# Performance work log

Hardware: AMD Instinct MI355X
Metric: run time of the kernel (lower is better)

Reference implementation:

```python
import jax, jax.numpy as jnp
import numpy as np

N_FILTERS = 40
FILTER_SIZE = 401   # int(16000*25/1000), forced odd
POOL_STRIDE = 160   # int(16000*10/1000)
EPS = 1e-6
S_SMOOTH = 0.04     # fixed PCEN smoothing coefficient s
DELTA = 2.0         # fixed PCEN bias delta
R_MIN, R_MAX = 0.2, 1.0
HIDDEN = 32


def setup_inputs() -> dict:
    key = jax.random.key(0)
    ks = jax.random.split(key, 6)
    B, L = 8, 160000
    x = jax.random.normal(ks[0], (B, L), dtype=jnp.float32)
    # mel-initialized Gabor params (as in mel_filter_params)
    sr, fmin, fmax = 16000.0, 60.0, 7800.0
    min_mel = 1127.0 * np.log1p(fmin / 700.0)
    max_mel = 1127.0 * np.log1p(fmax / 700.0)
    peaks_mel = np.linspace(min_mel, max_mel, N_FILTERS + 2)
    peaks_hz = 700.0 * np.expm1(peaks_mel / 1127.0)
    center_freqs = jnp.asarray(peaks_hz[1:-1] * 2.0 * np.pi / sr, dtype=jnp.float32)
    z = np.sqrt(2.0 * np.log(2.0)) / np.pi
    bandwidths = jnp.asarray(z * sr / (peaks_hz[2:] - peaks_hz[:-2]), dtype=jnp.float32)
    pooling_widths = jnp.full((N_FILTERS,), 0.4, dtype=jnp.float32)
    # GRU (input_size=1, hidden=32) + head Linear(32,32)->ReLU->Linear(32,2)
    def gl(k, shape):
        return jax.random.normal(k, shape, dtype=jnp.float32) * 0.1
    w_ih = gl(ks[1], (3 * HIDDEN, 1))
    w_hh = gl(ks[2], (3 * HIDDEN, HIDDEN))
    b_ih = jnp.zeros((3 * HIDDEN,), jnp.float32)
    b_hh = jnp.zeros((3 * HIDDEN,), jnp.float32)
    hw1 = gl(ks[3], (32, HIDDEN)); hb1 = jnp.zeros((32,), jnp.float32)
    hw2 = gl(ks[4], (2, 32)); hb2 = jnp.zeros((2,), jnp.float32)
    return dict(x=x, center_freqs=center_freqs, bandwidths=bandwidths,
                pooling_widths=pooling_widths, w_ih=w_ih, w_hh=w_hh,
                b_ih=b_ih, b_hh=b_hh, hw1=hw1, hb1=hb1, hw2=hw2, hb2=hb2)


def _gabor_filterbank(x, center_freqs, bandwidths, pooling_widths):
    z = np.sqrt(2.0 * np.log(2.0)) / np.pi
    cf = jnp.clip(center_freqs, 0.0, np.pi)
    bw = jnp.clip(bandwidths, 4.0 * z, FILTER_SIZE * z)
    t = jnp.arange(-(FILTER_SIZE // 2), (FILTER_SIZE + 1) // 2, dtype=jnp.float32)
    denom = 1.0 / (jnp.sqrt(2.0 * np.pi) * bw)                        # [F]
    gauss = jnp.exp(-(t[None, :] ** 2) / (2.0 * bw[:, None] ** 2))    # [F,K]
    phase = cf[:, None] * t[None, :]                                  # [F,K]
    fr = denom[:, None] * gauss * jnp.cos(phase)
    fi = denom[:, None] * gauss * jnp.sin(phase)
    filt = jnp.concatenate([fr, fi], axis=0)[:, None, :]              # [2F,1,K]
    pad = FILTER_SIZE // 2
    y = jax.lax.conv_general_dilated(x[:, None, :], filt, (1,), [(pad, pad)])
    y = y ** 2
    y = y[:, :N_FILTERS] + y[:, N_FILTERS:]                           # squared modulus [B,F,L]
    pw = jnp.clip(pooling_widths, 2.0 / FILTER_SIZE, 0.5)
    tt = jnp.arange(FILTER_SIZE, dtype=jnp.float32) / (FILTER_SIZE - 1) - 0.5
    win = jnp.exp(-0.5 * (tt[None, :] / pw[:, None]) ** 2)[:, None, :]  # [F,1,K]
    y = jax.lax.conv_general_dilated(y, win, (POOL_STRIDE,), [(pad, pad)],
                                     feature_group_count=N_FILTERS)
    return y  # [B,F,T]


def _gru_cell(h, xin, w_ih, w_hh, b_ih, b_hh):
    gi = xin @ w_ih.T + b_ih   # [N,3H]
    gh = h @ w_hh.T + b_hh
    i_r, i_z, i_n = jnp.split(gi, 3, axis=-1)
    h_r, h_z, h_n = jnp.split(gh, 3, axis=-1)
    r = jax.nn.sigmoid(i_r + h_r)
    zz = jax.nn.sigmoid(i_z + h_z)
    n = jnp.tanh(i_n + r * h_n)
    return (1.0 - zz) * n + zz * h


def _adaptive_pcen(frames, w_ih, w_hh, b_ih, b_hh, hw1, hb1, hw2, hb2):
    B, F, T = frames.shape
    Xt = jnp.transpose(frames, (2, 0, 1))  # [T,B,F]

    def controller(x_prev, x_t):  # each [B,F] -> per-bin (alpha, r)
        xp = x_prev.reshape(-1, 1)
        xc = x_t.reshape(-1, 1)
        h = jnp.zeros((B * F, HIDDEN), frames.dtype)
        h = _gru_cell(h, xp, w_ih, w_hh, b_ih, b_hh)
        h = _gru_cell(h, xc, w_ih, w_hh, b_ih, b_hh)
        hid = jax.nn.relu(h @ hw1.T + hb1)
        logits = hid @ hw2.T + hb2  # [B*F,2]
        alpha = jax.nn.sigmoid(logits[:, 0]).reshape(B, F)
        r = (R_MIN + (R_MAX - R_MIN) * jax.nn.sigmoid(logits[:, 1])).reshape(B, F)
        return alpha, r

    def step(carry, X_t):
        M_prev, X_prev = carry
        alpha, r = controller(X_prev, X_t)
        M_t = (1.0 - S_SMOOTH) * M_prev + S_SMOOTH * X_t
        out = (X_t / (M_t + EPS) ** alpha + DELTA) ** r - DELTA ** r
        return (M_t, X_t), out

    init = (jnp.zeros((B, F), frames.dtype), Xt[0])
    _, outs = jax.lax.scan(step, init, Xt)
    return jnp.transpose(outs, (1, 2, 0))  # [B,F,T]


def reference(x, center_freqs, bandwidths, pooling_widths,
              w_ih, w_hh, b_ih, b_hh, hw1, hb1, hw2, hb2):
    frames = _gabor_filterbank(x, center_freqs, bandwidths, pooling_widths)
    return _adaptive_pcen(frames, w_ih, w_hh, b_ih, b_hh, hw1, hb1, hw2, hb2)
```

## Files before the change

kernel.cpp:

```cpp
#include <hip/hip_runtime.h>
#include <math.h>

#define NF 40
#define FS 401
#define AST 424
#define PSTRIDE 160
#define BB 8
#define LL 160000
#define PADL 256
#define LST 161024
#define TOUT 1000
#define NTILE 512
#define NCHUNKC 313
#define ROWCH 121
#define ROWST (ROWCH*8)
#define EROW 520
#define TCP 16
#define NCHUNKP 63
#define NCONVB 5032

typedef __attribute__((ext_vector_type(8))) _Float16 half8v;
typedef __attribute__((ext_vector_type(4))) _Float16 half4v;
typedef __attribute__((ext_vector_type(4))) float float4v;
typedef _Float16 f16;

__device__ __forceinline__ float sigm(float x) { return 1.0f / (1.0f + __expf(-x)); }
__device__ __forceinline__ float tanh_fast(float x) { return 1.0f - 2.0f / (__expf(2.0f * x) + 1.0f); }

__global__ __launch_bounds__(256) void prep_all(
    const float* __restrict__ x, const float* __restrict__ cf_,
    const float* __restrict__ bw_, f16* __restrict__ xb, f16* __restrict__ Ag)
{
    int blk = blockIdx.x;
    if (blk < NCONVB) {
        int i = blk * 256 + threadIdx.x;
        int b = i / LST, o = i % LST;
        float v = 0.0f;
        if (o >= PADL && o < PADL + LL) v = x[b * LL + (o - PADL)];
        xb[i] = (f16)v;
        return;
    }
    const float PI_F = 3.14159265358979323846f;
    int row = blk - NCONVB;
    int f = row >> 1, comp = row & 1;
    float Z = sqrtf(2.0f * logf(2.0f)) / PI_F;
    float cf = fminf(fmaxf(cf_[f], 0.0f), PI_F);
    float bw = fminf(fmaxf(bw_[f], 4.0f * Z), 401.0f * Z);
    float denom = 1.0f / (sqrtf(2.0f * PI_F) * bw);
    float inv2 = 1.0f / (2.0f * bw * bw);
    for (int k = threadIdx.x; k < AST; k += 256) {
        float v = 0.0f;
        if (k < FS) {
            float t = (float)(k - 200);
            float g = denom * expf(-(t * t) * inv2);
            float sv, cv;
            sincosf(cf * t, &sv, &cv);
            v = comp ? g * sv : g * cv;
        }
        Ag[row * AST + k] = (f16)v;
    }
}

__global__ __launch_bounds__(256, 2) void conv_mfma(
    const f16* __restrict__ xb,
    const f16* __restrict__ Ag,
    f16* __restrict__ eb)
{
    __shared__ __align__(16) unsigned char smem[40 * EROW * 2];
    f16* slab = (f16*)smem;
    f16* eL   = (f16*)smem;

    int chunk = blockIdx.x;
    int bi = blockIdx.y;
    int p0 = chunk * NTILE;
    int pbase = PADL + p0 - 200;
    const f16* xs = xb + (size_t)bi * LST;
    int tid = threadIdx.x;

    for (int sc = tid; sc < 8 * 120; sc += 256) {
        int r = sc / 120, m = sc - r * 120;
        int s0 = pbase + 8 * m + (r & ~1);
        const uint* gp = (const uint*)(xs + s0);
        uint v0 = gp[0], v1 = gp[1], v2 = gp[2], v3 = gp[3], v4 = gp[4];
        if (r & 1) {
            v0 = __builtin_amdgcn_alignbyte(v1, v0, 2);
            v1 = __builtin_amdgcn_alignbyte(v2, v1, 2);
            v2 = __builtin_amdgcn_alignbyte(v3, v2, 2);
            v3 = __builtin_amdgcn_alignbyte(v4, v3, 2);
        }
        *(uint4*)(&slab[r * ROWST + 8 * m]) = make_uint4(v0, v1, v2, v3);
    }
    __syncthreads();

    int wv = tid >> 6, lane = tid & 63, q = lane >> 4, l15 = lane & 15;

    float4v acc[5][8];
#pragma unroll
    for (int t = 0; t < 5; ++t)
#pragma unroll
        for (int s = 0; s < 8; ++s)
            acc[t][s] = (float4v){0.f, 0.f, 0.f, 0.f};

    const f16* aP[5];
    const f16* bPtr[10];
#pragma unroll
    for (int t = 0; t < 5; ++t) aP[t] = Ag + (16 * t + l15) * AST + 8 * q;
#pragma unroll
    for (int s = 0; s < 10; ++s) {
        int pos = 128 * wv + 16 * s + l15;
        bPtr[s] = slab + (pos & 7) * ROWST + 8 * ((pos >> 3) + q);
    }

    half8v bf[8];
#pragma unroll
    for (int s = 0; s < 8; ++s) bf[s] = *(const half8v*)(bPtr[s]);

#pragma unroll
    for (int kk = 0; kk < 13; ++kk) {
        int k = 32 * kk;
        half8v af[5];
#pragma unroll
        for (int t = 0; t < 5; ++t) af[t] = *(const half8v*)(aP[t] + k);
        half8v nb0, nb1;
        if (kk < 12) {
            nb0 = *(const half8v*)(bPtr[8] + k);
            nb1 = *(const half8v*)(bPtr[9] + k);
        }
#pragma unroll
        for (int t = 0; t < 5; ++t)
#pragma unroll
            for (int s = 0; s < 8; ++s)
                acc[t][s] = __builtin_amdgcn_mfma_f32_16x16x32_f16(af[t], bf[s], acc[t][s], 0, 0, 0);
        if (kk < 12) {
#pragma unroll
            for (int s = 0; s < 6; ++s) bf[s] = bf[s + 2];
            bf[6] = nb0; bf[7] = nb1;
        }
    }

    __syncthreads();

#pragma unroll
    for (int t = 0; t < 5; ++t) {
        int f0 = 8 * t + 2 * q;
#pragma unroll
        for (int s = 0; s < 8; ++s) {
            float4v a = acc[t][s];
            int pl = 128 * wv + 16 * s + l15;
            eL[f0 * EROW + pl] = (f16)(a.x * a.x + a.y * a.y);
            eL[(f0 + 1) * EROW + pl] = (f16)(a.z * a.z + a.w * a.w);
        }
    }
    __syncthreads();

    f16* ebb = eb + (size_t)bi * NF * LL;
#pragma unroll
    for (int it = 0; it < 10; ++it) {
        int idx = it * 256 + tid;
        int row = idx >> 6;
        int off = (idx & 63) * 8;
        if (p0 + off < LL) {
            uint4 v = *(const uint4*)(&eL[row * EROW + off]);
            *(uint4*)(&ebb[row * LL + p0 + off]) = v;
        }
    }
}

__global__ __launch_bounds__(256) void pool_kernel(
    const f16* __restrict__ eb, const float* __restrict__ pw_, float* __restrict__ Xout)
{
    __shared__ float ys[2816];
    __shared__ float win[416];
    int chunk = blockIdx.x;
    int f = blockIdx.y;
    int bi = blockIdx.z;
    int tau0 = chunk * TCP;
    int start = tau0 * PSTRIDE - 200;
    int tid = threadIdx.x;

    float pw = fminf(fmaxf(pw_[f], 2.0f / 401.0f), 0.5f);
    float invpw = 1.0f / pw;
    for (int k = tid; k < 416; k += 256) {
        float w = 0.0f;
        if (k < FS) {
            float tt = (float)k * (1.0f / 400.0f) - 0.5f;
            float u = tt * invpw;
            w = expf(-0.5f * u * u);
        }
        win[k] = w;
    }
    const f16* erow = eb + ((size_t)bi * NF + f) * LL;
    if (start >= 0 && start + 2816 <= LL) {
        for (int j = tid; j < 352; j += 256) {
            half8v v = *(const half8v*)(erow + start + 8 * j);
#pragma unroll
            for (int i = 0; i < 8; ++i) ys[8 * j + i] = (float)v[i];
        }
    } else {
        for (int j = tid; j < 2816; j += 256) {
            int p = start + j;
            ys[j] = (p >= 0 && p < LL) ? (float)erow[p] : 0.0f;
        }
    }
    __syncthreads();

    int ft = tid >> 4, l16 = tid & 15;
    float acc = 0.0f;
    int yo = ft * PSTRIDE;
    for (int kw = l16; kw < FS; kw += 16)
        acc += ys[yo + kw] * win[kw];
#pragma unroll
    for (int off = 8; off > 0; off >>= 1)
        acc += __shfl_down(acc, off, 16);
    int tau = tau0 + ft;
    if (l16 == 0 && tau < TOUT)
        Xout[((size_t)bi * NF + f) * TOUT + tau] = acc;
}

__global__ __launch_bounds__(256) void pcen_scan_kernel(
    const float* __restrict__ X, float* __restrict__ M)
{
    int wid = (blockIdx.x * 256 + threadIdx.x) >> 6;
    int lane = threadIdx.x & 63;
    if (wid >= BB * NF) return;
    const float a1 = 0.96f;
    const float a2 = a1 * a1;
    const float a4 = a2 * a2;
    const float a8 = a4 * a4;
    const float a16 = a8 * a8;
    const float a32 = a16 * a16;
    const float ss = 0.04f;
    float al1 = powf(a1, (float)(lane + 1));
    float carry = 0.0f;
    const float* row = X + wid * TOUT;
    float* mrow = M + wid * TOUT;

    for (int c = 0; c < TOUT; c += 64) {
        int t = c + lane;
        float v = (t < TOUT) ? row[t] : 0.0f;
        float y = ss * v;
        float u;
        u = __shfl_up(y, 1, 64);  if (lane >= 1)  y = fmaf(a1, u, y);
        u = __shfl_up(y, 2, 64);  if (lane >= 2)  y = fmaf(a2, u, y);
        u = __shfl_up(y, 4, 64);  if (lane >= 4)  y = fmaf(a4, u, y);
        u = __shfl_up(y, 8, 64);  if (lane >= 8)  y = fmaf(a8, u, y);
        u = __shfl_up(y, 16, 64); if (lane >= 16) y = fmaf(a16, u, y);
        u = __shfl_up(y, 32, 64); if (lane >= 32) y = fmaf(a32, u, y);
        y = fmaf(al1, carry, y);
        carry = __shfl(y, 63, 64);
        if (t < TOUT) mrow[t] = y;
    }
}

__global__ __launch_bounds__(256) void pcen_ctrl_mfma(
    const float* __restrict__ X, const float* __restrict__ M,
    const float* __restrict__ w_ih, const float* __restrict__ w_hh,
    const float* __restrict__ b_ih, const float* __restrict__ b_hh,
    const float* __restrict__ hw1, const float* __restrict__ hb1,
    const float* __restrict__ hw2, const float* __restrict__ hb2,
    float* __restrict__ out)
{
    __shared__ f16 s_whhA[96 * 40];
    __shared__ f16 s_w1A[32 * 40];
    __shared__ __align__(16) float4 s_A1[32];
    __shared__ __align__(16) float4 s_A2[32];
    __shared__ float s_hb1[32];
    __shared__ float s_hw2[64];
    __shared__ float s_hb2[2];
    __shared__ f16 sh1[4][16 * 40];
    __shared__ f16 sh2[4][16 * 40];
    __shared__ float sxc[4][16], sxp[4][16], smv[4][16];

    int tid = threadIdx.x;
    for (int i = tid; i < 96 * 32; i += 256) {
        int m = i >> 5, k = i & 31;
        s_whhA[m * 40 + k] = (f16)w_hh[i];
    }
    for (int i = tid; i < 32 * 32; i += 256) {
        int m = i >> 5, k = i & 31;
        s_w1A[m * 40 + k] = (f16)hw1[i];
    }
    if (tid < 32) {
        int j = tid;
        s_A1[j] = make_float4(w_ih[j], b_ih[j] + b_hh[j],
                              w_ih[32 + j], b_ih[32 + j] + b_hh[32 + j]);
        s_A2[j] = make_float4(w_ih[64 + j], b_ih[64 + j], b_hh[64 + j], 0.0f);
        s_hb1[j] = hb1[j];
    }
    if (tid < 64) s_hw2[tid] = hw2[tid];
    if (tid < 2)  s_hb2[tid] = hb2[tid];
    __syncthreads();

    int wv = tid >> 6, lane = tid & 63;
    int c = lane & 15, q = lane >> 4;
    int instBase = blockIdx.x * 64 + wv * 16;

    if (lane < 16) {
        int idx = instBase + lane;
        int t = idx % TOUT;
        float xcv = X[idx];
        float xpv = (t == 0) ? xcv : X[idx - 1];
        sxc[wv][lane] = xcv;
        sxp[wv][lane] = xpv;
        smv[wv][lane] = M[idx];
    }
    float xp = sxp[wv][c];
    float xc = sxc[wv][c];
    float mv = smv[wv][c];

    float h1v[8];
#pragma unroll
    for (int jj = 0; jj < 8; ++jj) {
        int j = (jj < 4) ? (4 * q + jj) : (16 + 4 * q + (jj - 4));
        float4 a1 = s_A1[j];
        float4 a2 = s_A2[j];
        float r = sigm(fmaf(xp, a1.x, a1.y));
        float z = sigm(fmaf(xp, a1.z, a1.w));
        float n = tanh_fast(fmaf(xp, a2.x, a2.y) + r * a2.z);
        h1v[jj] = (1.0f - z) * n;
    }

    {
        half4v lo = {(f16)h1v[0], (f16)h1v[1], (f16)h1v[2], (f16)h1v[3]};
        half4v hi = {(f16)h1v[4], (f16)h1v[5], (f16)h1v[6], (f16)h1v[7]};
        *(half4v*)(&sh1[wv][c * 40 + 4 * q]) = lo;
        *(half4v*)(&sh1[wv][c * 40 + 16 + 4 * q]) = hi;
    }

    float4v acc[6];
    {
        half8v bf = *(const half8v*)(&sh1[wv][c * 40 + 8 * q]);
#pragma unroll
        for (int t = 0; t < 6; ++t) {
            half8v af = *(const half8v*)(&s_whhA[(16 * t + c) * 40 + 8 * q]);
            acc[t] = __builtin_amdgcn_mfma_f32_16x16x32_f16(af, bf, (float4v){0.f,0.f,0.f,0.f}, 0, 0, 0);
        }
    }

    float h2v[8];
#pragma unroll
    for (int jj = 0; jj < 8; ++jj) {
        int j = (jj < 4) ? (4 * q + jj) : (16 + 4 * q + (jj - 4));
        int reg = jj & 3;
        float accR = (jj < 4) ? acc[0][reg] : acc[1][reg];
        float accZ = (jj < 4) ? acc[2][reg] : acc[3][reg];
        float accN = (jj < 4) ? acc[4][reg] : acc[5][reg];
        float4 a1 = s_A1[j];
        float4 a2 = s_A2[j];
        float r = sigm(fmaf(xc, a1.x, a1.y) + accR);
        float z = sigm(fmaf(xc, a1.z, a1.w) + accZ);
        float gn = accN + a2.z;
        float n = tanh_fast(fmaf(xc, a2.x, a2.y) + r * gn);
        h2v[jj] = fmaf(z, h1v[jj] - n, n);
    }

    {
        half4v lo = {(f16)h2v[0], (f16)h2v[1], (f16)h2v[2], (f16)h2v[3]};
        half4v hi = {(f16)h2v[4], (f16)h2v[5], (f16)h2v[6], (f16)h2v[7]};
        *(half4v*)(&sh2[wv][c * 40 + 4 * q]) = lo;
        *(half4v*)(&sh2[wv][c * 40 + 16 + 4 * q]) = hi;
    }

    float4v hacc[2];
    {
        half8v bf = *(const half8v*)(&sh2[wv][c * 40 + 8 * q]);
#pragma unroll
        for (int t = 0; t < 2; ++t) {
            half8v af = *(const half8v*)(&s_w1A[(16 * t + c) * 40 + 8 * q]);
            hacc[t] = __builtin_amdgcn_mfma_f32_16x16x32_f16(af, bf, (float4v){0.f,0.f,0.f,0.f}, 0, 0, 0);
        }
    }

    float p0 = 0.f, p1 = 0.f;
#pragma unroll
    for (int jj = 0; jj < 8; ++jj) {
        int i = (jj < 4) ? (4 * q + jj) : (16 + 4 * q + (jj - 4));
        int reg = jj & 3;
        float hv = (jj < 4) ? hacc[0][reg] : hacc[1][reg];
        hv = fmaxf(hv + s_hb1[i], 0.0f);
        p0 = fmaf(hv, s_hw2[i], p0);
        p1 = fmaf(hv, s_hw2[32 + i], p1);
    }
    p0 += __shfl_xor(p0, 16);
    p0 += __shfl_xor(p0, 32);
    p1 += __shfl_xor(p1, 16);
    p1 += __shfl_xor(p1, 32);

    float alpha = sigm(p0 + s_hb2[0]);
    float rr = fmaf(0.8f, sigm(p1 + s_hb2[1]), 0.2f);
    float md = __expf(alpha * __logf(mv + 1e-6f));
    float bse = xc / md + 2.0f;
    float val = __expf(rr * __logf(bse)) - __expf(rr * 0.69314718056f);
    if (lane < 16)
        out[instBase + lane] = val;
}

extern "C" void kernel_launch(void* const* d_in, const int* in_sizes, int n_in,
                              void* d_out, int out_size, void* d_ws, size_t ws_size,
                              hipStream_t stream) {
    const float* x    = (const float*)d_in[0];
    const float* cf   = (const float*)d_in[1];
    const float* bw   = (const float*)d_in[2];
    const float* pw   = (const float*)d_in[3];
    const float* w_ih = (const float*)d_in[4];
    const float* w_hh = (const float*)d_in[5];
    const float* b_ih = (const float*)d_in[6];
    const float* b_hh = (const float*)d_in[7];
    const float* hw1  = (const float*)d_in[8];
    const float* hb1  = (const float*)d_in[9];
    const float* hw2  = (const float*)d_in[10];
    const float* hb2  = (const float*)d_in[11];
    float* out = (float*)d_out;

    const size_t xb_b = (size_t)BB * LST * 2;
    const size_t ag_b = (size_t)80 * AST * 2;
    const size_t xm_b = (size_t)2 * BB * NF * TOUT * 4;
    size_t fixed = xb_b + ag_b + xm_b;
    size_t e_per_batch = (size_t)NF * LL * 2;
    int nb;
    if (ws_size >= fixed + 8 * e_per_batch)      nb = 8;
    else if (ws_size >= fixed + 2 * e_per_batch) nb = 2;
    else                                         nb = 1;
    int nslice = BB / nb;

    f16* xb   = (f16*)d_ws;
    f16* Ag   = xb + (size_t)BB * LST;
    f16* ebuf = Ag + (size_t)80 * AST;
    float* Xf = (float*)(ebuf + (size_t)nb * NF * LL);
    float* Mf = Xf + (size_t)BB * NF * TOUT;

    prep_all<<<dim3(NCONVB + 80), dim3(256), 0, stream>>>(x, cf, bw, xb, Ag);

    for (int sl = 0; sl < nslice; ++sl) {
        conv_mfma<<<dim3(NCHUNKC, nb), dim3(256), 0, stream>>>(
            xb + (size_t)sl * nb * LST, Ag, ebuf);
        pool_kernel<<<dim3(NCHUNKP, NF, nb), dim3(256), 0, stream>>>(
            ebuf, pw, Xf + (size_t)sl * nb * NF * TOUT);
    }

    pcen_scan_kernel<<<dim3((BB * NF * 64) / 256), dim3(256), 0, stream>>>(Xf, Mf);
    pcen_ctrl_mfma<<<dim3((BB * NF * TOUT) / 64), dim3(256), 0, stream>>>(
        Xf, Mf, w_ih, w_hh, b_ih, b_hh, hw1, hb1, hw2, hb2, out);
}
```

Before: 259.8 us.

## Fuse Gaussian pooling into conv kernel with two-slot partial sums

The separate pooling kernel is removed. Each conv block now pools its own energy tile from LDS against a precomputed pooling window table, and writes partial sums into one of two slots chosen by chunk parity. The PCEN scan kernel then adds the slot partials into the pooled frames. This drops the large fp16 energy round trip through global memory and the batch-slicing loop. In exchange, the conv blocks do some extra pooling work and the frame boundary logic gets more complex.

Result: slower. 351.2 us (+35.2%).

```diff
diff --git a/kernel.cpp b/kernel.cpp
--- a/kernel.cpp
+++ b/kernel.cpp
@@ -14,13 +14,13 @@
 #define NCHUNKC 313
 #define ROWCH 121
 #define ROWST (ROWCH*8)
-#define EROW 520
-#define TCP 16
-#define NCHUNKP 63
+#define EROW 528
+#define WLEN 416
 #define NCONVB 5032
 
 typedef __attribute__((ext_vector_type(8))) _Float16 half8v;
 typedef __attribute__((ext_vector_type(4))) _Float16 half4v;
+typedef __attribute__((ext_vector_type(2))) _Float16 half2v;
 typedef __attribute__((ext_vector_type(4))) float float4v;
 typedef _Float16 f16;
 
@@ -29,7 +29,8 @@
 
 __global__ __launch_bounds__(256) void prep_all(
     const float* __restrict__ x, const float* __restrict__ cf_,
-    const float* __restrict__ bw_, f16* __restrict__ xb, f16* __restrict__ Ag)
+    const float* __restrict__ bw_, const float* __restrict__ pw_,
+    f16* __restrict__ xb, f16* __restrict__ Ag, float* __restrict__ Wg)
 {
     int blk = blockIdx.x;
     if (blk < NCONVB) {
@@ -40,31 +41,47 @@
         xb[i] = (f16)v;
         return;
     }
-    const float PI_F = 3.14159265358979323846f;
-    int row = blk - NCONVB;
-    int f = row >> 1, comp = row & 1;
-    float Z = sqrtf(2.0f * logf(2.0f)) / PI_F;
-    float cf = fminf(fmaxf(cf_[f], 0.0f), PI_F);
-    float bw = fminf(fmaxf(bw_[f], 4.0f * Z), 401.0f * Z);
-    float denom = 1.0f / (sqrtf(2.0f * PI_F) * bw);
-    float inv2 = 1.0f / (2.0f * bw * bw);
-    for (int k = threadIdx.x; k < AST; k += 256) {
-        float v = 0.0f;
+    if (blk < NCONVB + 80) {
+        const float PI_F = 3.14159265358979323846f;
+        int row = blk - NCONVB;
+        int f = row >> 1, comp = row & 1;
+        float Z = sqrtf(2.0f * logf(2.0f)) / PI_F;
+        float cf = fminf(fmaxf(cf_[f], 0.0f), PI_F);
+        float bw = fminf(fmaxf(bw_[f], 4.0f * Z), 401.0f * Z);
+        float denom = 1.0f / (sqrtf(2.0f * PI_F) * bw);
+        float inv2 = 1.0f / (2.0f * bw * bw);
+        for (int k = threadIdx.x; k < AST; k += 256) {
+            float v = 0.0f;
+            if (k < FS) {
+                float t = (float)(k - 200);
+                float g = denom * expf(-(t * t) * inv2);
+                float sv, cv;
+                sincosf(cf * t, &sv, &cv);
+                v = comp ? g * sv : g * cv;
+            }
+            Ag[row * AST + k] = (f16)v;
+        }
+        return;
+    }
+    int f = blk - (NCONVB + 80);
+    float pw = fminf(fmaxf(pw_[f], 2.0f / 401.0f), 0.5f);
+    float invpw = 1.0f / pw;
+    for (int k = threadIdx.x; k < WLEN; k += 256) {
+        float w = 0.0f;
         if (k < FS) {
-            float t = (float)(k - 200);
-            float g = denom * expf(-(t * t) * inv2);
-            float sv, cv;
-            sincosf(cf * t, &sv, &cv);
-            v = comp ? g * sv : g * cv;
-        }
-        Ag[row * AST + k] = (f16)v;
+            float ttv = (float)k * (1.0f / 400.0f) - 0.5f;
+            float u = ttv * invpw;
+            w = expf(-0.5f * u * u);
+        }
+        Wg[f * WLEN + k] = w;
     }
 }
 
-__global__ __launch_bounds__(256, 2) void conv_mfma(
+__global__ __launch_bounds__(256, 2) void conv_pool(
     const f16* __restrict__ xb,
     const f16* __restrict__ Ag,
-    f16* __restrict__ eb)
+    const float* __restrict__ Wg,
+    float* __restrict__ Pp)
 {
     __shared__ __align__(16) unsigned char smem[40 * EROW * 2];
     f16* slab = (f16*)smem;
@@ -147,78 +164,63 @@
         for (int s = 0; s < 8; ++s) {
             float4v a = acc[t][s];
             int pl = 128 * wv + 16 * s + l15;
-            eL[f0 * EROW + pl] = (f16)(a.x * a.x + a.y * a.y);
-            eL[(f0 + 1) * EROW + pl] = (f16)(a.z * a.z + a.w * a.w);
-        }
+            bool ok = (p0 + pl) < LL;
+            eL[f0 * EROW + pl] = ok ? (f16)(a.x * a.x + a.y * a.y) : (f16)0.f;
+            eL[(f0 + 1) * EROW + pl] = ok ? (f16)(a.z * a.z + a.w * a.w) : (f16)0.f;
+        }
+    }
+    for (int i = tid; i < 40 * 16; i += 256) {
+        int r = i >> 4, cc = 512 + (i & 15);
+        eL[r * EROW + cc] = (f16)0.f;
     }
     __syncthreads();
 
-    f16* ebb = eb + (size_t)bi * NF * LL;
-#pragma unroll
-    for (int it = 0; it < 10; ++it) {
-        int idx = it * 256 + tid;
-        int row = idx >> 6;
-        int off = (idx & 63) * 8;
-        if (p0 + off < LL) {
-            uint4 v = *(const uint4*)(&eL[row * EROW + off]);
-            *(uint4*)(&ebb[row * LL + p0 + off]) = v;
-        }
+    int tau_lo = (p0 - 41) / 160;
+    if (tau_lo < 0) tau_lo = 0;
+    int tau_hi = (p0 + 711) / 160;
+    if (tau_hi > TOUT - 1) tau_hi = TOUT - 1;
+    int ntau = tau_hi - tau_lo + 1;
+    int npr = ntau * 10;
+    int kwl = 2 * l15;
+    int slot = chunk & 1;
+
+    for (int pr = wv; pr < npr; pr += 4) {
+        int ta = pr / 10, fb = pr - ta * 10;
+        int tau = tau_lo + ta;
+        int base = tau * 160 - 200 - p0;
+        int lo = base < 0 ? -base : 0;
+        int hi = 512 - base; if (hi > 401) hi = 401;
+        int it0 = lo >> 5;
+        int it1 = (hi + 31) >> 5;
+        int f = 4 * fb + q;
+        const float* wrow = Wg + f * WLEN;
+        const f16* erow = eL + f * EROW;
+        float pa = 0.0f;
+#pragma unroll
+        for (int it = 0; it < 13; ++it) {
+            if (it >= it0 && it < it1) {
+                int kw = 32 * it + kwl;
+                bool v = (kw >= lo) && (kw < hi);
+                int plc = v ? (base + kw) : 0;
+                half2v ep = *(const half2v*)(erow + plc);
+                float2 w2 = *(const float2*)(wrow + kw);
+                if (v) {
+                    pa = fmaf((float)ep[0], w2.x, pa);
+                    pa = fmaf((float)ep[1], w2.y, pa);
+                }
+            }
+        }
+        pa += __shfl_xor(pa, 1);
+        pa += __shfl_xor(pa, 2);
+        pa += __shfl_xor(pa, 4);
+        pa += __shfl_xor(pa, 8);
+        if (l15 == 0)
+            Pp[(((size_t)bi * NF + f) * TOUT + tau) * 2 + slot] = pa;
     }
 }
 
-__global__ __launch_bounds__(256) void pool_kernel(
-    const f16* __restrict__ eb, const float* __restrict__ pw_, float* __restrict__ Xout)
-{
-    __shared__ float ys[2816];
-    __shared__ float win[416];
-    int chunk = blockIdx.x;
-    int f = blockIdx.y;
-    int bi = blockIdx.z;
-    int tau0 = chunk * TCP;
-    int start = tau0 * PSTRIDE - 200;
-    int tid = threadIdx.x;
-
-    float pw = fminf(fmaxf(pw_[f], 2.0f / 401.0f), 0.5f);
-    float invpw = 1.0f / pw;
-    for (int k = tid; k < 416; k += 256) {
-        float w = 0.0f;
-        if (k < FS) {
-            float tt = (float)k * (1.0f / 400.0f) - 0.5f;
-            float u = tt * invpw;
-            w = expf(-0.5f * u * u);
-        }
-        win[k] = w;
-    }
-    const f16* erow = eb + ((size_t)bi * NF + f) * LL;
-    if (start >= 0 && start + 2816 <= LL) {
-        for (int j = tid; j < 352; j += 256) {
-            half8v v = *(const half8v*)(erow + start + 8 * j);
-#pragma unroll
-            for (int i = 0; i < 8; ++i) ys[8 * j + i] = (float)v[i];
-        }
-    } else {
-        for (int j = tid; j < 2816; j += 256) {
-            int p = start + j;
-            ys[j] = (p >= 0 && p < LL) ? (float)erow[p] : 0.0f;
-        }
-    }
-    __syncthreads();
-
-    int ft = tid >> 4, l16 = tid & 15;
-    float acc = 0.0f;
-    int yo = ft * PSTRIDE;
-    for (int kw = l16; kw < FS; kw += 16)
-        acc += ys[yo + kw] * win[kw];
-#pragma unroll
-    for (int off = 8; off > 0; off >>= 1)
-        acc += __shfl_down(acc, off, 16);
-    int tau = tau0 + ft;
-    if (l16 == 0 && tau < TOUT)
-        Xout[((size_t)bi * NF + f) * TOUT + tau] = acc;
-}
-
 __global__ __launch_bounds__(256) void pcen_scan_kernel(
-    const float* __restrict__ X, float* __restrict__ M)
+    const float* __restrict__ Pp, float* __restrict__ X, float* __restrict__ M)
 {
     int wid = (blockIdx.x * 256 + threadIdx.x) >> 6;
     int lane = threadIdx.x & 63;
@@ -232,12 +234,22 @@
     const float ss = 0.04f;
     float al1 = powf(a1, (float)(lane + 1));
     float carry = 0.0f;
-    const float* row = X + wid * TOUT;
-    float* mrow = M + wid * TOUT;
+    const float* prow = Pp + (size_t)wid * TOUT * 2;
+    float* xrow = X + (size_t)wid * TOUT;
+    float* mrow = M + (size_t)wid * TOUT;
 
     for (int c = 0; c < TOUT; c += 64) {
         int t = c + lane;
-        float v = (t < TOUT) ? row[t] : 0.0f;
+        float v = 0.0f;
+        if (t < TOUT) {
+            int s = t * 160 - 200;
+            int cl = (s > 0) ? (s >> 9) : 0;
+            int ch = (s + 400) >> 9;
+            if (ch > NCHUNKC - 1) ch = NCHUNKC - 1;
+            v = prow[2 * t + (cl & 1)];
+            if (ch > cl) v += prow[2 * t + ((cl & 1) ^ 1)];
+            xrow[t] = v;
+        }
         float y = ss * v;
         float u;
         u = __shfl_up(y, 1, 64);  if (lane >= 1)  y = fmaf(a1, u, y);
@@ -412,33 +424,19 @@
     const float* hb2  = (const float*)d_in[11];
     float* out = (float*)d_out;
 
-    const size_t xb_b = (size_t)BB * LST * 2;
-    const size_t ag_b = (size_t)80 * AST * 2;
-    const size_t xm_b = (size_t)2 * BB * NF * TOUT * 4;
-    size_t fixed = xb_b + ag_b + xm_b;
-    size_t e_per_batch = (size_t)NF * LL * 2;
-    int nb;
-    if (ws_size >= fixed + 8 * e_per_batch)      nb = 8;
-    else if (ws_size >= fixed + 2 * e_per_batch) nb = 2;
-    else                                         nb = 1;
-    int nslice = BB / nb;
-
     f16* xb   = (f16*)d_ws;
     f16* Ag   = xb + (size_t)BB * LST;
-    f16* ebuf = Ag + (size_t)80 * AST;
-    float* Xf = (float*)(ebuf + (size_t)nb * NF * LL);
+    float* Wg = (float*)(Ag + (size_t)80 * AST);
+    float* Pp = Wg + (size_t)NF * WLEN;
+    float* Xf = Pp + (size_t)BB * NF * TOUT * 2;
     float* Mf = Xf + (size_t)BB * NF * TOUT;
 
-    prep_all<<<dim3(NCONVB + 80), dim3(256), 0, stream>>>(x, cf, bw, xb, Ag);
-
-    for (int sl = 0; sl < nslice; ++sl) {
-        conv_mfma<<<dim3(NCHUNKC, nb), dim3(256), 0, stream>>>(
-            xb + (size_t)sl * nb * LST, Ag, ebuf);
-        pool_kernel<<<dim3(NCHUNKP, NF, nb), dim3(256), 0, stream>>>(
-            ebuf, pw, Xf + (size_t)sl * nb * NF * TOUT);
-    }
-
-    pcen_scan_kernel<<<dim3((BB * NF * 64) / 256), dim3(256), 0, stream>>>(Xf, Mf);
+    prep_all<<<dim3(NCONVB + 80 + 40), dim3(256), 0, stream>>>(
+        x, cf, bw, pw, xb, Ag, Wg);
+
+    conv_pool<<<dim3(NCHUNKC, BB), dim3(256), 0, stream>>>(xb, Ag, Wg, Pp);
+
+    pcen_scan_kernel<<<dim3((BB * NF * 64) / 256), dim3(256), 0, stream>>>(Pp, Xf, Mf);
     pcen_ctrl_mfma<<<dim3((BB * NF * TOUT) / 64), dim3(256), 0, stream>>>(
         Xf, Mf, w_ih, w_hh, b_ih, b_hh, hw1, hb1, hw2, hb2, out);
 }
```
